# Optimization experiments

Measured on AMD Instinct MI355X. Metric: run time of the kernel, lower is better.

## Reference

```python
import jax, jax.numpy as jnp
import numpy as np

B, S, T, D = 4, 2, 1024, 512
H = 8
HD = D // H
EPS = 1e-6
LN_EPS = 1e-5


def setup_inputs() -> dict:
    key = jax.random.key(0)
    ks = jax.random.split(key, 12)
    def lin(k, fan_in, shape):
        bound = 1.0 / np.sqrt(fan_in)
        return jax.random.uniform(k, shape, jnp.float32, -bound, bound)
    return {
        "hidden_states": jax.random.normal(ks[0], (B, S, T, D), jnp.float32),
        "Wq": lin(ks[1], D, (D, D)), "bq": lin(ks[2], D, (D,)),
        "Wk": lin(ks[3], D, (D, D)), "bk": lin(ks[4], D, (D,)),
        "Wv": lin(ks[5], D, (D, D)), "bv": lin(ks[6], D, (D,)),
        "Wo": lin(ks[7], D, (D, D)), "bo": lin(ks[8], D, (D,)),
        "ln_g": jnp.ones((S, D), jnp.float32),
        "ln_b": jnp.zeros((S, D), jnp.float32),
        "gate_alpha": jnp.full((S,), 0.01, jnp.float32),
    }


def _heads(x):
    # [B,T,D] -> [B,H,T,HD]
    return x.reshape(B, T, H, HD).transpose(0, 2, 1, 3)


def _layernorm(x, g, b):
    mu = jnp.mean(x, axis=-1, keepdims=True)
    var = jnp.var(x, axis=-1, keepdims=True)
    return (x - mu) * jax.lax.rsqrt(var + LN_EPS) * g + b


def reference(hidden_states, Wq, bq, Wk, bk, Wv, bv, Wo, bo, ln_g, ln_b, gate_alpha):
    h1, h2 = hidden_states[:, 0], hidden_states[:, 1]  # [B,T,D]
    proj = lambda x, W, b: jnp.einsum('btd,ed->bte', x, W) + b
    Q1, K1, V1 = _heads(proj(h1, Wq, bq)), _heads(proj(h1, Wk, bk)), _heads(proj(h1, Wv, bv))
    Q2, K2, V2 = _heads(proj(h2, Wq, bq)), _heads(proj(h2, Wk, bk)), _heads(proj(h2, Wv, bv))
    scale = 1.0 / np.sqrt(HD)
    L12 = jnp.einsum('bhqd,bhkd->bhqk', Q1, K2) * scale
    L21 = jnp.einsum('bhqd,bhkd->bhqk', Q2, K1) * scale
    S12 = jax.nn.softmax(L12, axis=-1)
    S21 = jax.nn.softmax(L21, axis=-1)
    M = S12 + S21 + EPS
    A12 = S12 / M
    A21 = S21 / M
    H1 = jnp.einsum('bhqk,bhkd->bhqd', A12, V2).transpose(0, 2, 1, 3).reshape(B, T, D)
    H2 = jnp.einsum('bhqk,bhkd->bhqd', A21, V1).transpose(0, 2, 1, 3).reshape(B, T, D)
    H1 = _layernorm(jnp.einsum('btd,ed->bte', H1, Wo) + bo, ln_g[0], ln_b[0])
    H2 = _layernorm(jnp.einsum('btd,ed->bte', H2, Wo) + bo, ln_g[1], ln_b[1])
    attn = jnp.stack([H1, H2], axis=1)  # [B,2,T,D]
    return hidden_states + attn * gate_alpha[None, :, None, None]
```

## Files before the change

kernel.cpp:

```cpp
#include <hip/hip_runtime.h>

#define DEVI __device__ __forceinline__

typedef __bf16 v8bf __attribute__((ext_vector_type(8)));
typedef float  v4f  __attribute__((ext_vector_type(4)));
typedef short  v4s  __attribute__((ext_vector_type(4)));

DEVI unsigned short f2bf(float f) {
  unsigned u = __builtin_bit_cast(unsigned, f);
  u += 0x7fffu + ((u >> 16) & 1u);
  return (unsigned short)(u >> 16);
}
DEVI v4f MFMA32(v8bf a, v8bf b, v4f c) {
  return __builtin_amdgcn_mfma_f32_16x16x32_bf16(a, b, c, 0, 0, 0);
}
DEVI v8bf ldfrag(const unsigned short* p) {
  return __builtin_bit_cast(v8bf, *(const uint4*)p);
}
DEVI v4s ld4s(const unsigned short* p) {
  return __builtin_bit_cast(v4s, *(const uint2*)p);
}
DEVI unsigned pkbf(float lo, float hi) {
  unsigned a = __builtin_bit_cast(unsigned, hi) + 0x8000u;
  unsigned b = __builtin_bit_cast(unsigned, lo) + 0x8000u;
  return __builtin_amdgcn_perm(a, b, 0x07060302u);
}
DEVI float lo2f(unsigned u) { return __builtin_bit_cast(float, u << 16); }
DEVI float hi2f(unsigned u) { return __builtin_bit_cast(float, u & 0xffff0000u); }

#if __has_builtin(__builtin_amdgcn_exp2f)
DEVI float fexp2(float x) { return __builtin_amdgcn_exp2f(x); }
#else
DEVI float fexp2(float x) { return exp2f(x); }
#endif

#if __has_builtin(__builtin_amdgcn_mfma_f32_16x16x16bf16_1k)
#define HAVE_MFMA16 1
DEVI v4f MFMA16(v4s a, v4s b, v4f c) {
  return __builtin_amdgcn_mfma_f32_16x16x16bf16_1k(a, b, c, 0, 0, 0);
}
#else
#define HAVE_MFMA16 0
#endif

#if __has_builtin(__builtin_amdgcn_global_load_lds)
DEVI void g2l(const unsigned short* g, unsigned short* l) {
  __builtin_amdgcn_global_load_lds(
      (const __attribute__((address_space(1))) unsigned int*)g,
      (__attribute__((address_space(3))) unsigned int*)l, 16, 0, 0);
}
#else
DEVI void g2l(const unsigned short* g, unsigned short* l) {
  *(uint4*)((char*)l + (threadIdx.x & 63) * 16) = *(const uint4*)g;
}
#endif

__global__ __launch_bounds__(256) void convert_kernel(
    const float* __restrict__ X, const float* __restrict__ Wq,
    const float* __restrict__ Wk, const float* __restrict__ Wv,
    const float* __restrict__ Wo, unsigned short* __restrict__ dst)
{
  int t = blockIdx.x * 256 + threadIdx.x;
  int idx = t * 4;
  const float* src;
  if (idx < 4194304) {
    src = X + idx;
  } else {
    int u = idx - 4194304;
    int w = u >> 18;
    const float* W = (w == 0) ? Wq : (w == 1) ? Wk : (w == 2) ? Wv : Wo;
    src = W + (u & 262143);
  }
  float4 f = *(const float4*)src;
  uint2 o;
  o.x = pkbf(f.x, f.y);
  o.y = pkbf(f.z, f.w);
  *(uint2*)&dst[idx] = o;
}

template<int OUTM, int BM>
__global__ __launch_bounds__(256) void gemm_bt(
    const unsigned short* __restrict__ A,
    const unsigned short* __restrict__ W0, const unsigned short* __restrict__ W1,
    const unsigned short* __restrict__ W2,
    const float* __restrict__ b0, const float* __restrict__ b1, const float* __restrict__ b2,
    void* __restrict__ C0, void* __restrict__ C1, void* __restrict__ C2)
{
  const int K = 512, N = 512;
  const int MI = BM / 32;
  const int PER = (BM / 8 + 16) / 4;
  __shared__ unsigned short sAB[(BM + 128) * 64];
  const int z = blockIdx.z;
  const unsigned short* W = (z == 0) ? W0 : (z == 1) ? W1 : W2;
  const float* bias = (z == 0) ? b0 : (z == 1) ? b1 : b2;
  void* C = (z == 0) ? C0 : (z == 1) ? C1 : C2;

  const int tid = threadIdx.x;
  const int lane = tid & 63, wave = tid >> 6;
  const int l15 = lane & 15, quad = lane >> 4, swl = l15 & 7;
  const int lrow = lane >> 3;
  const int lc8 = ((lane & 7) ^ (lrow & 7)) * 8;
  const int wm = (wave >> 1) * (BM / 2), wn = (wave & 1) * 64;
  const int mbase = blockIdx.y * BM, nbase = blockIdx.x * 128;

  const unsigned short* gsrc[PER];
  unsigned short* ldst[PER];
#pragma unroll
  for (int t = 0; t < PER; t++) {
    int c = wave * PER + t;
    ldst[t] = &sAB[c * 512];
    if (c < BM / 8) gsrc[t] = A + (size_t)(mbase + c * 8 + lrow) * K + lc8;
    else            gsrc[t] = W + (size_t)(nbase + (c - BM / 8) * 8 + lrow) * K + lc8;
  }

  v4f acc[MI][4] = {};

  for (int kt = 0; kt < K; kt += 64) {
    __syncthreads();
#pragma unroll
    for (int t = 0; t < PER; t++) g2l(gsrc[t] + kt, ldst[t]);
    __syncthreads();
#pragma unroll
    for (int s = 0; s < 2; s++) {
      v8bf af[MI], bf[4];
#pragma unroll
      for (int i = 0; i < MI; i++)
        af[i] = ldfrag(&sAB[(wm + i * 16 + l15) * 64 + ((s * 4 + quad) ^ swl) * 8]);
#pragma unroll
      for (int j = 0; j < 4; j++)
        bf[j] = ldfrag(&sAB[(BM + wn + j * 16 + l15) * 64 + ((s * 4 + quad) ^ swl) * 8]);
#pragma unroll
      for (int i = 0; i < MI; i++)
#pragma unroll
        for (int j = 0; j < 4; j++)
          acc[i][j] = MFMA32(af[i], bf[j], acc[i][j]);
    }
  }

#pragma unroll
  for (int i = 0; i < MI; i++)
#pragma unroll
    for (int j = 0; j < 4; j++) {
      int row0 = mbase + wm + i * 16 + quad * 4;
      int col = nbase + wn + j * 16 + l15;
      float v[4];
#pragma unroll
      for (int r = 0; r < 4; r++) v[r] = acc[i][j][r] + bias[col];
      if (OUTM == 1) {
#pragma unroll
        for (int r = 0; r < 4; r++) ((float*)C)[(size_t)(row0 + r) * N + col] = v[r];
      } else if (z == 2) {
        int bs = row0 >> 10, t0 = row0 & 1023;
        int hh = col >> 6, hd = col & 63;
        uint2 o;
        o.x = pkbf(v[0], v[1]);
        o.y = pkbf(v[2], v[3]);
        *(uint2*)&((unsigned short*)C)[(size_t)((bs * 8 + hh) * 64 + hd) * 1024 + t0] = o;
      } else {
#pragma unroll
        for (int r = 0; r < 4; r++)
          ((unsigned short*)C)[(size_t)(row0 + r) * N + col] = f2bf(v[r]);
      }
    }
}

__global__ __launch_bounds__(256, 2) void attn_kernel(
    const unsigned short* __restrict__ Qg, const unsigned short* __restrict__ Kg,
    const unsigned short* __restrict__ VTg, unsigned short* __restrict__ Hc)
{
  __shared__ unsigned short sK[2][2][64][64];
  __shared__ unsigned short sV[2][2][64][64];

  const int pair = blockIdx.x & 31;
  const int b = pair >> 3, h = pair & 7;
  const int qt = blockIdx.x >> 5;
  const int tid = threadIdx.x;
  const int lane = tid & 63, wave = tid >> 6;
  const int l15 = lane & 15, quad = lane >> 4, swl = l15 & 7;
  const int lrow = lane >> 3;
  const int lc8 = ((lane & 7) ^ (lrow & 7)) * 8;
  const int qbase = qt * 64 + wave * 16;
  const float S2 = 0.125f * 1.44269504f;

  const unsigned short* kgp[2];
  const unsigned short* vgp[2];
#pragma unroll
  for (int st = 0; st < 2; st++) {
    kgp[st] = Kg + (size_t)((b * 2 + st) * 1024) * 512 + h * 64;
    vgp[st] = VTg + (size_t)(((b * 2 + st) * 8 + h) * 64) * 1024;
  }

  v8bf qf[2][2];
#pragma unroll
  for (int d = 0; d < 2; d++)
#pragma unroll
    for (int s = 0; s < 2; s++) {
      int qrow = (b * 2 + d) * 1024 + qbase + l15;
      qf[d][s] = ldfrag(&Qg[(size_t)qrow * 512 + h * 64 + s * 32 + quad * 8]);
    }

  float lacc[2] = {0.f, 0.f};
  {
    const unsigned short* gA[4];
    unsigned short* lA[2][4];
#pragma unroll
    for (int t = 0; t < 4; t++) {
      int c = wave * 4 + t;
      gA[t] = kgp[c >> 3] + (size_t)((c & 7) * 8 + lrow) * 512 + lc8;
      lA[0][t] = &sK[0][c >> 3][(c & 7) * 8][0];
      lA[1][t] = &sK[1][c >> 3][(c & 7) * 8][0];
    }
#pragma unroll
    for (int t = 0; t < 4; t++) g2l(gA[t], lA[0][t]);

    for (int kt = 0; kt < 16; kt++) {
      __syncthreads();
      if (kt < 15) {
#pragma unroll
        for (int t = 0; t < 4; t++)
          g2l(gA[t] + (size_t)(kt + 1) * 32768, lA[(kt + 1) & 1][t]);
      }
      const int bu = kt & 1;
      v4f acc[2][4] = {};
#pragma unroll
      for (int s = 0; s < 2; s++)
#pragma unroll
        for (int d = 0; d < 2; d++)
#pragma unroll
          for (int j = 0; j < 4; j++) {
            v8bf kf = ldfrag(&sK[bu][1 - d][j * 16 + l15][((s * 4 + quad) ^ swl) * 8]);
            acc[d][j] = MFMA32(kf, qf[d][s], acc[d][j]);
          }
#pragma unroll
      for (int d = 0; d < 2; d++)
#pragma unroll
        for (int j = 0; j < 4; j++)
#pragma unroll
          for (int r = 0; r < 4; r++)
            lacc[d] += fexp2(acc[d][j][r] * S2);
    }
  }
  float ll[2];
#pragma unroll
  for (int d = 0; d < 2; d++) {
    float v = lacc[d];
    v += __shfl_xor(v, 16);
    v += __shfl_xor(v, 32);
    ll[d] = __log2f(v);
  }
  const float dll = ll[0] - ll[1];

  v4f oacc[2][4] = {};
  {
    const unsigned short* gB[8];
    unsigned short* lB[2][8];
    size_t stp[8];
#pragma unroll
    for (int t = 0; t < 8; t++) {
      int c = wave * 8 + t;
      if (c < 16) {
        gB[t] = kgp[c >> 3] + (size_t)((c & 7) * 8 + lrow) * 512 + lc8;
        stp[t] = 32768;
        lB[0][t] = &sK[0][c >> 3][(c & 7) * 8][0];
        lB[1][t] = &sK[1][c >> 3][(c & 7) * 8][0];
      } else {
        int cv = c - 16;
        gB[t] = vgp[cv >> 3] + (size_t)((cv & 7) * 8 + lrow) * 1024 + lc8;
        stp[t] = 64;
        lB[0][t] = &sV[0][cv >> 3][(cv & 7) * 8][0];
        lB[1][t] = &sV[1][cv >> 3][(cv & 7) * 8][0];
      }
    }
    __syncthreads();
#pragma unroll
    for (int t = 0; t < 8; t++) g2l(gB[t], lB[0][t]);

    for (int kt = 0; kt < 16; kt++) {
      __syncthreads();
      if (kt < 15) {
#pragma unroll
        for (int t = 0; t < 8; t++)
          g2l(gB[t] + (size_t)(kt + 1) * stp[t], lB[(kt + 1) & 1][t]);
      }
      const int bu = kt & 1;

      v4f acc[2][4] = {};
#pragma unroll
      for (int s = 0; s < 2; s++)
#pragma unroll
        for (int d = 0; d < 2; d++)
#pragma unroll
          for (int j = 0; j < 4; j++) {
            v8bf kf = ldfrag(&sK[bu][1 - d][j * 16 + l15][((s * 4 + quad) ^ swl) * 8]);
            acc[d][j] = MFMA32(kf, qf[d][s], acc[d][j]);
          }

#pragma unroll
      for (int j = 0; j < 4; j++) {
        float r0[4], r1[4];
#pragma unroll
        for (int r = 0; r < 4; r++) {
          float t = fmaf(acc[1][j][r] - acc[0][j][r], S2, dll);
          float ri = __builtin_amdgcn_rcpf(1.f + fexp2(t));
          r0[r] = ri;
          r1[r] = 1.f - ri;
        }
#if HAVE_MFMA16
        uint2 w0, w1;
        w0.x = pkbf(r0[0], r0[1]); w0.y = pkbf(r0[2], r0[3]);
        w1.x = pkbf(r1[0], r1[1]); w1.y = pkbf(r1[2], r1[3]);
        v4s af0 = __builtin_bit_cast(v4s, w0);
        v4s af1 = __builtin_bit_cast(v4s, w1);
        int vcol = ((j * 2 + (quad >> 1)) ^ swl) * 8 + (quad & 1) * 4;
#pragma unroll
        for (int nt = 0; nt < 4; nt++) {
          v4s vf0 = ld4s(&sV[bu][1][nt * 16 + l15][vcol]);
          v4s vf1 = ld4s(&sV[bu][0][nt * 16 + l15][vcol]);
          oacc[0][nt] = MFMA16(af0, vf0, oacc[0][nt]);
          oacc[1][nt] = MFMA16(af1, vf1, oacc[1][nt]);
        }
#else
#pragma unroll
        for (int d = 0; d < 2; d++) {
          float (&cb)[4] = (d == 0) ? r0 : r1;
          v8bf a;
#pragma unroll
          for (int jj = 0; jj < 8; jj++) {
            int src = l15 + 16 * ((jj >> 2) + (quad & 1) * 2);
            float v = __shfl(cb[jj & 3], src);
            a[jj] = __builtin_bit_cast(__bf16, f2bf(v));
          }
#pragma unroll
          for (int nt = 0; nt < 4; nt++) {
            v8bf vf = ldfrag(&sV[bu][1 - d][nt * 16 + l15]
                               [(((j & 2) * 2 + quad) ^ swl) * 8]);
            oacc[d][nt] = MFMA32(a, vf, oacc[d][nt]);
          }
        }
#endif
      }
    }
  }

#pragma unroll
  for (int d = 0; d < 2; d++)
#pragma unroll
    for (int nt = 0; nt < 4; nt++)
#pragma unroll
      for (int r = 0; r < 4; r++) {
        int row = (b * 2 + d) * 1024 + qbase + quad * 4 + r;
        int col = h * 64 + nt * 16 + l15;
        Hc[(size_t)row * 512 + col] = f2bf(oacc[d][nt][r]);
      }
}

__global__ __launch_bounds__(256) void ln_kernel(
    const unsigned short* __restrict__ Pb, const float* __restrict__ hidden,
    const float* __restrict__ ln_g, const float* __restrict__ ln_b,
    const float* __restrict__ gate, float* __restrict__ out)
{
  const int row = blockIdx.x * 4 + (threadIdx.x >> 6);
  const int s = (row >> 10) & 1;
  const int lane = threadIdx.x & 63;
  const int d0 = lane * 8;

  uint4 up = *(const uint4*)&Pb[(size_t)row * 512 + d0];
  float x[8] = { lo2f(up.x), hi2f(up.x), lo2f(up.y), hi2f(up.y),
                 lo2f(up.z), hi2f(up.z), lo2f(up.w), hi2f(up.w) };
  float s1 = 0.f, s2 = 0.f;
#pragma unroll
  for (int i = 0; i < 8; i++) { s1 += x[i]; s2 += x[i] * x[i]; }
#pragma unroll
  for (int m = 1; m < 64; m <<= 1) { s1 += __shfl_xor(s1, m); s2 += __shfl_xor(s2, m); }
  float mu = s1 * (1.f / 512.f);
  float var = s2 * (1.f / 512.f) - mu * mu;
  float rs = rsqrtf(var + 1e-5f);
  float al = gate[s];

  float4 h0 = *(const float4*)&hidden[(size_t)row * 512 + d0];
  float4 h1 = *(const float4*)&hidden[(size_t)row * 512 + d0 + 4];
  float4 g0 = *(const float4*)&ln_g[s * 512 + d0];
  float4 g1 = *(const float4*)&ln_g[s * 512 + d0 + 4];
  float4 bb0 = *(const float4*)&ln_b[s * 512 + d0];
  float4 bb1 = *(const float4*)&ln_b[s * 512 + d0 + 4];
  float4 o0, o1;
  o0.x = h0.x + ((x[0] - mu) * rs * g0.x + bb0.x) * al;
  o0.y = h0.y + ((x[1] - mu) * rs * g0.y + bb0.y) * al;
  o0.z = h0.z + ((x[2] - mu) * rs * g0.z + bb0.z) * al;
  o0.w = h0.w + ((x[3] - mu) * rs * g0.w + bb0.w) * al;
  o1.x = h1.x + ((x[4] - mu) * rs * g1.x + bb1.x) * al;
  o1.y = h1.y + ((x[5] - mu) * rs * g1.y + bb1.y) * al;
  o1.z = h1.z + ((x[6] - mu) * rs * g1.z + bb1.z) * al;
  o1.w = h1.w + ((x[7] - mu) * rs * g1.w + bb1.w) * al;
  *(float4*)&out[(size_t)row * 512 + d0] = o0;
  *(float4*)&out[(size_t)row * 512 + d0 + 4] = o1;
}

extern "C" void kernel_launch(void* const* d_in, const int* in_sizes, int n_in,
                              void* d_out, int out_size, void* d_ws, size_t ws_size,
                              hipStream_t stream)
{
  const float* hidden = (const float*)d_in[0];
  const float* Wq = (const float*)d_in[1];
  const float* bq = (const float*)d_in[2];
  const float* Wk = (const float*)d_in[3];
  const float* bk = (const float*)d_in[4];
  const float* Wv = (const float*)d_in[5];
  const float* bv = (const float*)d_in[6];
  const float* Wo = (const float*)d_in[7];
  const float* bo = (const float*)d_in[8];
  const float* ln_g = (const float*)d_in[9];
  const float* ln_b = (const float*)d_in[10];
  const float* gate = (const float*)d_in[11];

  unsigned short* U = (unsigned short*)d_ws;
  unsigned short* Xbf = U;
  unsigned short* Wqb = U + 4194304;
  unsigned short* Wkb = U + 4456448;
  unsigned short* Wvb = U + 4718592;
  unsigned short* Wob = U + 4980736;
  unsigned short* Qg  = U + 5242880;
  unsigned short* Kg  = U + 9437184;
  unsigned short* VT  = U + 13631488;
  unsigned short* Hc  = U + 17825792;
  unsigned short* Pb  = (unsigned short*)((char*)d_ws + 44302336);

  convert_kernel<<<dim3(5120), 256, 0, stream>>>(hidden, Wq, Wk, Wv, Wo, Xbf);
  gemm_bt<0, 128><<<dim3(4, 64, 3), 256, 0, stream>>>(Xbf, Wqb, Wkb, Wvb, bq, bk, bv, Qg, Kg, VT);
  attn_kernel<<<dim3(512), 256, 0, stream>>>(Qg, Kg, VT, Hc);
  gemm_bt<0, 64><<<dim3(4, 128, 1), 256, 0, stream>>>(Hc, Wob, Wob, Wob, bo, bo, bo, Pb, Pb, Pb);
  ln_kernel<<<dim3(2048), 256, 0, stream>>>(Pb, hidden, ln_g, ln_b, gate, (float*)d_out);
}
```

Measured before the change: 181.3 us.

## Split attention key tiles across two wave groups with 512-thread blocks

Doubles the attention block to 8 waves: each group of four waves handles half of each 64-key tile (j split by wj), so per-wave MFMA work and global-to-LDS copies are halved. Partial softmax denominators are combined through shared memory before the log, and partial output accumulators are reduced through LDS before the final store. This raises the number of waves per CU to better hide latency, at the cost of extra LDS reductions, extra barriers, and register pressure under the tighter launch bounds.

```diff
diff --git a/kernel.cpp b/kernel.cpp
--- a/kernel.cpp
+++ b/kernel.cpp
@@ -164,7 +164,7 @@
     }
 }
 
-__global__ __launch_bounds__(256, 2) void attn_kernel(
+__global__ __launch_bounds__(512, 4) void attn_kernel(
     const unsigned short* __restrict__ Qg, const unsigned short* __restrict__ Kg,
     const unsigned short* __restrict__ VTg, unsigned short* __restrict__ Hc)
 {
@@ -176,10 +176,11 @@
   const int qt = blockIdx.x >> 5;
   const int tid = threadIdx.x;
   const int lane = tid & 63, wave = tid >> 6;
+  const int wq = wave & 3, wj = wave >> 2;
   const int l15 = lane & 15, quad = lane >> 4, swl = l15 & 7;
   const int lrow = lane >> 3;
   const int lc8 = ((lane & 7) ^ (lrow & 7)) * 8;
-  const int qbase = qt * 64 + wave * 16;
+  const int qbase = qt * 64 + wq * 16;
   const float S2 = 0.125f * 1.44269504f;
 
   const unsigned short* kgp[2];
@@ -201,63 +202,69 @@
 
   float lacc[2] = {0.f, 0.f};
   {
-    const unsigned short* gA[4];
-    unsigned short* lA[2][4];
-#pragma unroll
-    for (int t = 0; t < 4; t++) {
-      int c = wave * 4 + t;
+    const unsigned short* gA[2];
+    unsigned short* lA[2][2];
+#pragma unroll
+    for (int t = 0; t < 2; t++) {
+      int c = wave * 2 + t;
       gA[t] = kgp[c >> 3] + (size_t)((c & 7) * 8 + lrow) * 512 + lc8;
       lA[0][t] = &sK[0][c >> 3][(c & 7) * 8][0];
       lA[1][t] = &sK[1][c >> 3][(c & 7) * 8][0];
     }
 #pragma unroll
-    for (int t = 0; t < 4; t++) g2l(gA[t], lA[0][t]);
+    for (int t = 0; t < 2; t++) g2l(gA[t], lA[0][t]);
 
     for (int kt = 0; kt < 16; kt++) {
       __syncthreads();
       if (kt < 15) {
 #pragma unroll
-        for (int t = 0; t < 4; t++)
+        for (int t = 0; t < 2; t++)
           g2l(gA[t] + (size_t)(kt + 1) * 32768, lA[(kt + 1) & 1][t]);
       }
       const int bu = kt & 1;
-      v4f acc[2][4] = {};
+      v4f acc[2][2] = {};
 #pragma unroll
       for (int s = 0; s < 2; s++)
 #pragma unroll
         for (int d = 0; d < 2; d++)
 #pragma unroll
-          for (int j = 0; j < 4; j++) {
+          for (int jl = 0; jl < 2; jl++) {
+            int j = wj * 2 + jl;
             v8bf kf = ldfrag(&sK[bu][1 - d][j * 16 + l15][((s * 4 + quad) ^ swl) * 8]);
-            acc[d][j] = MFMA32(kf, qf[d][s], acc[d][j]);
+            acc[d][jl] = MFMA32(kf, qf[d][s], acc[d][jl]);
           }
 #pragma unroll
       for (int d = 0; d < 2; d++)
 #pragma unroll
-        for (int j = 0; j < 4; j++)
+        for (int jl = 0; jl < 2; jl++)
 #pragma unroll
           for (int r = 0; r < 4; r++)
-            lacc[d] += fexp2(acc[d][j][r] * S2);
-    }
-  }
-  float ll[2];
-#pragma unroll
-  for (int d = 0; d < 2; d++) {
-    float v = lacc[d];
-    v += __shfl_xor(v, 16);
-    v += __shfl_xor(v, 32);
-    ll[d] = __log2f(v);
-  }
-  const float dll = ll[0] - ll[1];
+            lacc[d] += fexp2(acc[d][jl][r] * S2);
+    }
+  }
+  float dll;
+  {
+    float* redA = (float*)sV;
+    float v0 = lacc[0];
+    v0 += __shfl_xor(v0, 16); v0 += __shfl_xor(v0, 32);
+    float v1 = lacc[1];
+    v1 += __shfl_xor(v1, 16); v1 += __shfl_xor(v1, 32);
+    redA[wave * 128 + lane] = v0;
+    redA[wave * 128 + 64 + lane] = v1;
+    __syncthreads();
+    float s0 = v0 + redA[(wave ^ 4) * 128 + lane];
+    float s1 = v1 + redA[(wave ^ 4) * 128 + 64 + lane];
+    dll = __log2f(s0) - __log2f(s1);
+  }
 
   v4f oacc[2][4] = {};
   {
-    const unsigned short* gB[8];
-    unsigned short* lB[2][8];
-    size_t stp[8];
-#pragma unroll
-    for (int t = 0; t < 8; t++) {
-      int c = wave * 8 + t;
+    const unsigned short* gB[4];
+    unsigned short* lB[2][4];
+    size_t stp[4];
+#pragma unroll
+    for (int t = 0; t < 4; t++) {
+      int c = wave * 4 + t;
       if (c < 16) {
         gB[t] = kgp[c >> 3] + (size_t)((c & 7) * 8 + lrow) * 512 + lc8;
         stp[t] = 32768;
@@ -273,34 +280,36 @@
     }
     __syncthreads();
 #pragma unroll
-    for (int t = 0; t < 8; t++) g2l(gB[t], lB[0][t]);
+    for (int t = 0; t < 4; t++) g2l(gB[t], lB[0][t]);
 
     for (int kt = 0; kt < 16; kt++) {
       __syncthreads();
       if (kt < 15) {
 #pragma unroll
-        for (int t = 0; t < 8; t++)
+        for (int t = 0; t < 4; t++)
           g2l(gB[t] + (size_t)(kt + 1) * stp[t], lB[(kt + 1) & 1][t]);
       }
       const int bu = kt & 1;
 
-      v4f acc[2][4] = {};
+      v4f acc[2][2] = {};
 #pragma unroll
       for (int s = 0; s < 2; s++)
 #pragma unroll
         for (int d = 0; d < 2; d++)
 #pragma unroll
-          for (int j = 0; j < 4; j++) {
+          for (int jl = 0; jl < 2; jl++) {
+            int j = wj * 2 + jl;
             v8bf kf = ldfrag(&sK[bu][1 - d][j * 16 + l15][((s * 4 + quad) ^ swl) * 8]);
-            acc[d][j] = MFMA32(kf, qf[d][s], acc[d][j]);
+            acc[d][jl] = MFMA32(kf, qf[d][s], acc[d][jl]);
           }
 
 #pragma unroll
-      for (int j = 0; j < 4; j++) {
+      for (int jl = 0; jl < 2; jl++) {
+        const int j = wj * 2 + jl;
         float r0[4], r1[4];
 #pragma unroll
         for (int r = 0; r < 4; r++) {
-          float t = fmaf(acc[1][j][r] - acc[0][j][r], S2, dll);
+          float t = fmaf(acc[1][jl][r] - acc[0][jl][r], S2, dll);
           float ri = __builtin_amdgcn_rcpf(1.f + fexp2(t));
           r0[r] = ri;
           r1[r] = 1.f - ri;
@@ -342,16 +351,33 @@
     }
   }
 
-#pragma unroll
-  for (int d = 0; d < 2; d++)
-#pragma unroll
-    for (int nt = 0; nt < 4; nt++)
-#pragma unroll
-      for (int r = 0; r < 4; r++) {
-        int row = (b * 2 + d) * 1024 + qbase + quad * 4 + r;
-        int col = h * 64 + nt * 16 + l15;
-        Hc[(size_t)row * 512 + col] = f2bf(oacc[d][nt][r]);
-      }
+  __syncthreads();
+  {
+    float* red = (float*)sK;
+    if (wj == 1) {
+#pragma unroll
+      for (int d = 0; d < 2; d++)
+#pragma unroll
+        for (int nt = 0; nt < 4; nt++)
+#pragma unroll
+          for (int r = 0; r < 4; r++)
+            red[((d * 4 + nt) * 4 + r) * 256 + wq * 64 + lane] = oacc[d][nt][r];
+    }
+    __syncthreads();
+    if (wj == 0) {
+#pragma unroll
+      for (int d = 0; d < 2; d++)
+#pragma unroll
+        for (int nt = 0; nt < 4; nt++)
+#pragma unroll
+          for (int r = 0; r < 4; r++) {
+            float v = oacc[d][nt][r] + red[((d * 4 + nt) * 4 + r) * 256 + wq * 64 + lane];
+            int row = (b * 2 + d) * 1024 + qbase + quad * 4 + r;
+            int col = h * 64 + nt * 16 + l15;
+            Hc[(size_t)row * 512 + col] = f2bf(v);
+          }
+    }
+  }
 }
 
 __global__ __launch_bounds__(256) void ln_kernel(
@@ -427,7 +453,7 @@
 
   convert_kernel<<<dim3(5120), 256, 0, stream>>>(hidden, Wq, Wk, Wv, Wo, Xbf);
   gemm_bt<0, 128><<<dim3(4, 64, 3), 256, 0, stream>>>(Xbf, Wqb, Wkb, Wvb, bq, bk, bv, Qg, Kg, VT);
-  attn_kernel<<<dim3(512), 256, 0, stream>>>(Qg, Kg, VT, Hc);
+  attn_kernel<<<dim3(512), 512, 0, stream>>>(Qg, Kg, VT, Hc);
   gemm_bt<0, 64><<<dim3(4, 128, 1), 256, 0, stream>>>(Hc, Wob, Wob, Wob, bo, bo, bo, Pb, Pb, Pb);
   ln_kernel<<<dim3(2048), 256, 0, stream>>>(Pb, hidden, ln_g, ln_b, gate, (float*)d_out);
 }
```

Measured after the change: 180.5 us. Within noise of the previous version (-0.4%).

## Read V fragments directly from global memory and raise attention occupancy

Applied to the files above, without the earlier changes.

Removes the shared-memory staging buffer for V in the attention kernel. The PV MFMAs now load their V^T fragments straight from global memory (through L1/L2), and only K is prefetched into LDS. This halves LDS use, which allows the launch bound to rise from 2 to 3 blocks per CU and cuts the async copy traffic per iteration. In exchange, V loads become uncoalesced, latency-exposed global reads inside the inner loop, and the higher occupancy target may tighten the register budget.

```diff
diff --git a/kernel.cpp b/kernel.cpp
--- a/kernel.cpp
+++ b/kernel.cpp
@@ -164,12 +164,11 @@
     }
 }
 
-__global__ __launch_bounds__(256, 2) void attn_kernel(
+__global__ __launch_bounds__(256, 3) void attn_kernel(
     const unsigned short* __restrict__ Qg, const unsigned short* __restrict__ Kg,
     const unsigned short* __restrict__ VTg, unsigned short* __restrict__ Hc)
 {
   __shared__ unsigned short sK[2][2][64][64];
-  __shared__ unsigned short sV[2][2][64][64];
 
   const int pair = blockIdx.x & 31;
   const int b = pair >> 3, h = pair & 7;
@@ -199,17 +198,18 @@
       qf[d][s] = ldfrag(&Qg[(size_t)qrow * 512 + h * 64 + s * 32 + quad * 8]);
     }
 
+  const unsigned short* gA[4];
+  unsigned short* lA[2][4];
+#pragma unroll
+  for (int t = 0; t < 4; t++) {
+    int c = wave * 4 + t;
+    gA[t] = kgp[c >> 3] + (size_t)((c & 7) * 8 + lrow) * 512 + lc8;
+    lA[0][t] = &sK[0][c >> 3][(c & 7) * 8][0];
+    lA[1][t] = &sK[1][c >> 3][(c & 7) * 8][0];
+  }
+
   float lacc[2] = {0.f, 0.f};
   {
-    const unsigned short* gA[4];
-    unsigned short* lA[2][4];
-#pragma unroll
-    for (int t = 0; t < 4; t++) {
-      int c = wave * 4 + t;
-      gA[t] = kgp[c >> 3] + (size_t)((c & 7) * 8 + lrow) * 512 + lc8;
-      lA[0][t] = &sK[0][c >> 3][(c & 7) * 8][0];
-      lA[1][t] = &sK[1][c >> 3][(c & 7) * 8][0];
-    }
 #pragma unroll
     for (int t = 0; t < 4; t++) g2l(gA[t], lA[0][t]);
 
@@ -252,35 +252,21 @@
 
   v4f oacc[2][4] = {};
   {
-    const unsigned short* gB[8];
-    unsigned short* lB[2][8];
-    size_t stp[8];
-#pragma unroll
-    for (int t = 0; t < 8; t++) {
-      int c = wave * 8 + t;
-      if (c < 16) {
-        gB[t] = kgp[c >> 3] + (size_t)((c & 7) * 8 + lrow) * 512 + lc8;
-        stp[t] = 32768;
-        lB[0][t] = &sK[0][c >> 3][(c & 7) * 8][0];
-        lB[1][t] = &sK[1][c >> 3][(c & 7) * 8][0];
-      } else {
-        int cv = c - 16;
-        gB[t] = vgp[cv >> 3] + (size_t)((cv & 7) * 8 + lrow) * 1024 + lc8;
-        stp[t] = 64;
-        lB[0][t] = &sV[0][cv >> 3][(cv & 7) * 8][0];
-        lB[1][t] = &sV[1][cv >> 3][(cv & 7) * 8][0];
-      }
-    }
     __syncthreads();
 #pragma unroll
-    for (int t = 0; t < 8; t++) g2l(gB[t], lB[0][t]);
+    for (int t = 0; t < 4; t++) g2l(gA[t], lA[0][t]);
+
+    const unsigned short* vln[2];
+#pragma unroll
+    for (int st = 0; st < 2; st++)
+      vln[st] = vgp[st] + (size_t)l15 * 1024 + (quad >> 1) * 8 + (quad & 1) * 4;
 
     for (int kt = 0; kt < 16; kt++) {
       __syncthreads();
       if (kt < 15) {
 #pragma unroll
-        for (int t = 0; t < 8; t++)
-          g2l(gB[t] + (size_t)(kt + 1) * stp[t], lB[(kt + 1) & 1][t]);
+        for (int t = 0; t < 4; t++)
+          g2l(gA[t] + (size_t)(kt + 1) * 32768, lA[(kt + 1) & 1][t]);
       }
       const int bu = kt & 1;
 
@@ -311,11 +297,11 @@
         w1.x = pkbf(r1[0], r1[1]); w1.y = pkbf(r1[2], r1[3]);
         v4s af0 = __builtin_bit_cast(v4s, w0);
         v4s af1 = __builtin_bit_cast(v4s, w1);
-        int vcol = ((j * 2 + (quad >> 1)) ^ swl) * 8 + (quad & 1) * 4;
+        const int vofs = kt * 64 + j * 16;
 #pragma unroll
         for (int nt = 0; nt < 4; nt++) {
-          v4s vf0 = ld4s(&sV[bu][1][nt * 16 + l15][vcol]);
-          v4s vf1 = ld4s(&sV[bu][0][nt * 16 + l15][vcol]);
+          v4s vf0 = ld4s(vln[1] + (size_t)nt * 16384 + vofs);
+          v4s vf1 = ld4s(vln[0] + (size_t)nt * 16384 + vofs);
           oacc[0][nt] = MFMA16(af0, vf0, oacc[0][nt]);
           oacc[1][nt] = MFMA16(af1, vf1, oacc[1][nt]);
         }
@@ -332,8 +318,8 @@
           }
 #pragma unroll
           for (int nt = 0; nt < 4; nt++) {
-            v8bf vf = ldfrag(&sV[bu][1 - d][nt * 16 + l15]
-                               [(((j & 2) * 2 + quad) ^ swl) * 8]);
+            v8bf vf = ldfrag(vgp[1 - d] + (size_t)(nt * 16 + l15) * 1024 +
+                             kt * 64 + ((j & 2) * 2 + quad) * 8);
             oacc[d][nt] = MFMA32(a, vf, oacc[d][nt]);
           }
         }
```

Measured after the change: 266.5 us. 47.0% more time.

## Process two query row-groups per wave in attention to reuse K/V fragments

Applied to the files above, without the earlier changes.

The attention kernel now launches 128 threads (2 waves) per block instead of 256, and each wave handles 32 query rows as two 16-row groups. Every K fragment read from LDS feeds two MFMAs, and every V fragment feeds four, which halves LDS fragment traffic per FLOP. The cost is each wave issuing twice as many global-to-LDS copies, doubled accumulator registers (launch bounds relaxed to (128,1)), and fewer waves per block to hide latency.

```diff
diff --git a/kernel.cpp b/kernel.cpp
--- a/kernel.cpp
+++ b/kernel.cpp
@@ -164,7 +164,7 @@
     }
 }
 
-__global__ __launch_bounds__(256, 2) void attn_kernel(
+__global__ __launch_bounds__(128, 1) void attn_kernel(
     const unsigned short* __restrict__ Qg, const unsigned short* __restrict__ Kg,
     const unsigned short* __restrict__ VTg, unsigned short* __restrict__ Hc)
 {
@@ -179,7 +179,6 @@
   const int l15 = lane & 15, quad = lane >> 4, swl = l15 & 7;
   const int lrow = lane >> 3;
   const int lc8 = ((lane & 7) ^ (lrow & 7)) * 8;
-  const int qbase = qt * 64 + wave * 16;
   const float S2 = 0.125f * 1.44269504f;
 
   const unsigned short* kgp[2];
@@ -190,38 +189,40 @@
     vgp[st] = VTg + (size_t)(((b * 2 + st) * 8 + h) * 64) * 1024;
   }
 
-  v8bf qf[2][2];
-#pragma unroll
-  for (int d = 0; d < 2; d++)
-#pragma unroll
-    for (int s = 0; s < 2; s++) {
-      int qrow = (b * 2 + d) * 1024 + qbase + l15;
-      qf[d][s] = ldfrag(&Qg[(size_t)qrow * 512 + h * 64 + s * 32 + quad * 8]);
-    }
-
-  float lacc[2] = {0.f, 0.f};
+  v8bf qf[2][2][2];
+#pragma unroll
+  for (int g = 0; g < 2; g++)
+#pragma unroll
+    for (int d = 0; d < 2; d++)
+#pragma unroll
+      for (int s = 0; s < 2; s++) {
+        int qrow = (b * 2 + d) * 1024 + qt * 64 + wave * 32 + g * 16 + l15;
+        qf[g][d][s] = ldfrag(&Qg[(size_t)qrow * 512 + h * 64 + s * 32 + quad * 8]);
+      }
+
+  float lacc[2][2] = {};
   {
-    const unsigned short* gA[4];
-    unsigned short* lA[2][4];
-#pragma unroll
-    for (int t = 0; t < 4; t++) {
-      int c = wave * 4 + t;
+    const unsigned short* gA[8];
+    unsigned short* lA[2][8];
+#pragma unroll
+    for (int t = 0; t < 8; t++) {
+      int c = wave * 8 + t;
       gA[t] = kgp[c >> 3] + (size_t)((c & 7) * 8 + lrow) * 512 + lc8;
       lA[0][t] = &sK[0][c >> 3][(c & 7) * 8][0];
       lA[1][t] = &sK[1][c >> 3][(c & 7) * 8][0];
     }
 #pragma unroll
-    for (int t = 0; t < 4; t++) g2l(gA[t], lA[0][t]);
+    for (int t = 0; t < 8; t++) g2l(gA[t], lA[0][t]);
 
     for (int kt = 0; kt < 16; kt++) {
       __syncthreads();
       if (kt < 15) {
 #pragma unroll
-        for (int t = 0; t < 4; t++)
+        for (int t = 0; t < 8; t++)
           g2l(gA[t] + (size_t)(kt + 1) * 32768, lA[(kt + 1) & 1][t]);
       }
       const int bu = kt & 1;
-      v4f acc[2][4] = {};
+      v4f acc[2][2][4] = {};
 #pragma unroll
       for (int s = 0; s < 2; s++)
 #pragma unroll
@@ -229,35 +230,39 @@
 #pragma unroll
           for (int j = 0; j < 4; j++) {
             v8bf kf = ldfrag(&sK[bu][1 - d][j * 16 + l15][((s * 4 + quad) ^ swl) * 8]);
-            acc[d][j] = MFMA32(kf, qf[d][s], acc[d][j]);
-          }
-#pragma unroll
-      for (int d = 0; d < 2; d++)
-#pragma unroll
-        for (int j = 0; j < 4; j++)
-#pragma unroll
-          for (int r = 0; r < 4; r++)
-            lacc[d] += fexp2(acc[d][j][r] * S2);
-    }
-  }
-  float ll[2];
-#pragma unroll
-  for (int d = 0; d < 2; d++) {
-    float v = lacc[d];
-    v += __shfl_xor(v, 16);
-    v += __shfl_xor(v, 32);
-    ll[d] = __log2f(v);
-  }
-  const float dll = ll[0] - ll[1];
-
-  v4f oacc[2][4] = {};
+#pragma unroll
+            for (int g = 0; g < 2; g++)
+              acc[g][d][j] = MFMA32(kf, qf[g][d][s], acc[g][d][j]);
+          }
+#pragma unroll
+      for (int g = 0; g < 2; g++)
+#pragma unroll
+        for (int d = 0; d < 2; d++)
+#pragma unroll
+          for (int j = 0; j < 4; j++)
+#pragma unroll
+            for (int r = 0; r < 4; r++)
+              lacc[g][d] += fexp2(acc[g][d][j][r] * S2);
+    }
+  }
+  float dll[2];
+#pragma unroll
+  for (int g = 0; g < 2; g++) {
+    float v0 = lacc[g][0];
+    v0 += __shfl_xor(v0, 16); v0 += __shfl_xor(v0, 32);
+    float v1 = lacc[g][1];
+    v1 += __shfl_xor(v1, 16); v1 += __shfl_xor(v1, 32);
+    dll[g] = __log2f(v0) - __log2f(v1);
+  }
+
+  v4f oacc[2][2][4] = {};
   {
-    const unsigned short* gB[8];
-    unsigned short* lB[2][8];
-    size_t stp[8];
-#pragma unroll
-    for (int t = 0; t < 8; t++) {
-      int c = wave * 8 + t;
+    const unsigned short* gB[16];
+    unsigned short* lB[2][16];
+    size_t stp[16];
+#pragma unroll
+    for (int t = 0; t < 16; t++) {
+      int c = wave * 16 + t;
       if (c < 16) {
         gB[t] = kgp[c >> 3] + (size_t)((c & 7) * 8 + lrow) * 512 + lc8;
         stp[t] = 32768;
@@ -273,18 +278,18 @@
     }
     __syncthreads();
 #pragma unroll
-    for (int t = 0; t < 8; t++) g2l(gB[t], lB[0][t]);
+    for (int t = 0; t < 16; t++) g2l(gB[t], lB[0][t]);
 
     for (int kt = 0; kt < 16; kt++) {
       __syncthreads();
       if (kt < 15) {
 #pragma unroll
-        for (int t = 0; t < 8; t++)
+        for (int t = 0; t < 16; t++)
           g2l(gB[t] + (size_t)(kt + 1) * stp[t], lB[(kt + 1) & 1][t]);
       }
       const int bu = kt & 1;
 
-      v4f acc[2][4] = {};
+      v4f acc[2][2][4] = {};
 #pragma unroll
       for (int s = 0; s < 2; s++)
 #pragma unroll
@@ -292,49 +297,69 @@
 #pragma unroll
           for (int j = 0; j < 4; j++) {
             v8bf kf = ldfrag(&sK[bu][1 - d][j * 16 + l15][((s * 4 + quad) ^ swl) * 8]);
-            acc[d][j] = MFMA32(kf, qf[d][s], acc[d][j]);
+#pragma unroll
+            for (int g = 0; g < 2; g++)
+              acc[g][d][j] = MFMA32(kf, qf[g][d][s], acc[g][d][j]);
           }
 
 #pragma unroll
       for (int j = 0; j < 4; j++) {
-        float r0[4], r1[4];
-#pragma unroll
-        for (int r = 0; r < 4; r++) {
-          float t = fmaf(acc[1][j][r] - acc[0][j][r], S2, dll);
-          float ri = __builtin_amdgcn_rcpf(1.f + fexp2(t));
-          r0[r] = ri;
-          r1[r] = 1.f - ri;
+#if HAVE_MFMA16
+        v4s af0[2], af1[2];
+#pragma unroll
+        for (int g = 0; g < 2; g++) {
+          float r0[4], r1[4];
+#pragma unroll
+          for (int r = 0; r < 4; r++) {
+            float t = fmaf(acc[g][1][j][r] - acc[g][0][j][r], S2, dll[g]);
+            float ri = __builtin_amdgcn_rcpf(1.f + fexp2(t));
+            r0[r] = ri;
+            r1[r] = 1.f - ri;
+          }
+          uint2 w0, w1;
+          w0.x = pkbf(r0[0], r0[1]); w0.y = pkbf(r0[2], r0[3]);
+          w1.x = pkbf(r1[0], r1[1]); w1.y = pkbf(r1[2], r1[3]);
+          af0[g] = __builtin_bit_cast(v4s, w0);
+          af1[g] = __builtin_bit_cast(v4s, w1);
         }
-#if HAVE_MFMA16
-        uint2 w0, w1;
-        w0.x = pkbf(r0[0], r0[1]); w0.y = pkbf(r0[2], r0[3]);
-        w1.x = pkbf(r1[0], r1[1]); w1.y = pkbf(r1[2], r1[3]);
-        v4s af0 = __builtin_bit_cast(v4s, w0);
-        v4s af1 = __builtin_bit_cast(v4s, w1);
-        int vcol = ((j * 2 + (quad >> 1)) ^ swl) * 8 + (quad & 1) * 4;
+        const int vcol = ((j * 2 + (quad >> 1)) ^ swl) * 8 + (quad & 1) * 4;
 #pragma unroll
         for (int nt = 0; nt < 4; nt++) {
           v4s vf0 = ld4s(&sV[bu][1][nt * 16 + l15][vcol]);
           v4s vf1 = ld4s(&sV[bu][0][nt * 16 + l15][vcol]);
-          oacc[0][nt] = MFMA16(af0, vf0, oacc[0][nt]);
-          oacc[1][nt] = MFMA16(af1, vf1, oacc[1][nt]);
+#pragma unroll
+          for (int g = 0; g < 2; g++) {
+            oacc[g][0][nt] = MFMA16(af0[g], vf0, oacc[g][0][nt]);
+            oacc[g][1][nt] = MFMA16(af1[g], vf1, oacc[g][1][nt]);
+          }
         }
 #else
 #pragma unroll
-        for (int d = 0; d < 2; d++) {
-          float (&cb)[4] = (d == 0) ? r0 : r1;
-          v8bf a;
-#pragma unroll
-          for (int jj = 0; jj < 8; jj++) {
-            int src = l15 + 16 * ((jj >> 2) + (quad & 1) * 2);
-            float v = __shfl(cb[jj & 3], src);
-            a[jj] = __builtin_bit_cast(__bf16, f2bf(v));
-          }
-#pragma unroll
-          for (int nt = 0; nt < 4; nt++) {
-            v8bf vf = ldfrag(&sV[bu][1 - d][nt * 16 + l15]
-                               [(((j & 2) * 2 + quad) ^ swl) * 8]);
-            oacc[d][nt] = MFMA32(a, vf, oacc[d][nt]);
+        for (int g = 0; g < 2; g++) {
+          float r0[4], r1[4];
+#pragma unroll
+          for (int r = 0; r < 4; r++) {
+            float t = fmaf(acc[g][1][j][r] - acc[g][0][j][r], S2, dll[g]);
+            float ri = __builtin_amdgcn_rcpf(1.f + fexp2(t));
+            r0[r] = ri;
+            r1[r] = 1.f - ri;
+          }
+#pragma unroll
+          for (int d = 0; d < 2; d++) {
+            float (&cb)[4] = (d == 0) ? r0 : r1;
+            v8bf a;
+#pragma unroll
+            for (int jj = 0; jj < 8; jj++) {
+              int src = l15 + 16 * ((jj >> 2) + (quad & 1) * 2);
+              float v = __shfl(cb[jj & 3], src);
+              a[jj] = __builtin_bit_cast(__bf16, f2bf(v));
+            }
+#pragma unroll
+            for (int nt = 0; nt < 4; nt++) {
+              v8bf vf = ldfrag(&sV[bu][1 - d][nt * 16 + l15]
+                                 [(((j & 2) * 2 + quad) ^ swl) * 8]);
+              oacc[g][d][nt] = MFMA32(a, vf, oacc[g][d][nt]);
+            }
           }
         }
 #endif
@@ -343,15 +368,17 @@
   }
 
 #pragma unroll
-  for (int d = 0; d < 2; d++)
-#pragma unroll
-    for (int nt = 0; nt < 4; nt++)
-#pragma unroll
-      for (int r = 0; r < 4; r++) {
-        int row = (b * 2 + d) * 1024 + qbase + quad * 4 + r;
-        int col = h * 64 + nt * 16 + l15;
-        Hc[(size_t)row * 512 + col] = f2bf(oacc[d][nt][r]);
-      }
+  for (int g = 0; g < 2; g++)
+#pragma unroll
+    for (int d = 0; d < 2; d++)
+#pragma unroll
+      for (int nt = 0; nt < 4; nt++)
+#pragma unroll
+        for (int r = 0; r < 4; r++) {
+          int row = (b * 2 + d) * 1024 + qt * 64 + wave * 32 + g * 16 + quad * 4 + r;
+          int col = h * 64 + nt * 16 + l15;
+          Hc[(size_t)row * 512 + col] = f2bf(oacc[g][d][nt][r]);
+        }
 }
 
 __global__ __launch_bounds__(256) void ln_kernel(
@@ -427,7 +454,7 @@
 
   convert_kernel<<<dim3(5120), 256, 0, stream>>>(hidden, Wq, Wk, Wv, Wo, Xbf);
   gemm_bt<0, 128><<<dim3(4, 64, 3), 256, 0, stream>>>(Xbf, Wqb, Wkb, Wvb, bq, bk, bv, Qg, Kg, VT);
-  attn_kernel<<<dim3(512), 256, 0, stream>>>(Qg, Kg, VT, Hc);
+  attn_kernel<<<dim3(512), 128, 0, stream>>>(Qg, Kg, VT, Hc);
   gemm_bt<0, 64><<<dim3(4, 128, 1), 256, 0, stream>>>(Hc, Wob, Wob, Wob, bo, bo, bo, Pb, Pb, Pb);
   ln_kernel<<<dim3(2048), 256, 0, stream>>>(Pb, hidden, ln_g, ln_b, gate, (float*)d_out);
 }
```

After: 238.4 us. 31.5% more time.
